# Kernel optimization log

Measured on AMD Instinct MI355X. Metric: run time of the kernel, lower is better.

Reference implementation:

```python
import jax, jax.numpy as jnp
import numpy as np

N_NODES = 250_000
N_EDGES = 4_000_000


def setup_inputs() -> dict:
    key = jax.random.key(0)
    ks = jax.random.split(key, 8)
    x = jax.random.normal(ks[0], (N_NODES, 3), dtype=jnp.float32)
    w = jax.random.normal(ks[1], (N_EDGES, 4), dtype=jnp.float32)
    # MLP params: Linear(10->40), ReLU, Linear(40->4); torch Linear layout [out, in]
    W1 = jax.random.normal(ks[2], (40, 10), dtype=jnp.float32) * (1.0 / np.sqrt(10.0))
    b1 = jax.random.normal(ks[3], (40,), dtype=jnp.float32) * 0.01
    W2 = jax.random.normal(ks[4], (4, 40), dtype=jnp.float32) * (1.0 / np.sqrt(40.0))
    b2 = jax.random.normal(ks[5], (4,), dtype=jnp.float32) * 0.01
    src = jax.random.randint(ks[6], (N_EDGES,), 0, N_NODES, dtype=jnp.int64)
    dst = jax.random.randint(ks[7], (N_EDGES,), 0, N_NODES, dtype=jnp.int64)
    return {"x": x, "w": w, "W1": W1, "b1": b1, "W2": W2, "b2": b2,
            "src": src, "dst": dst}


def reference(x, w, W1, b1, W2, b2, src, dst):
    x_src = x[src]                                  # [E, 3] gather
    x_dst = x[dst]                                  # [E, 3] gather
    m = jnp.concatenate([x_src, x_dst, w], axis=1)  # [E, 10]
    h = jax.nn.relu(m @ W1.T + b1)                  # [E, 40]
    w_out = h @ W2.T + b2                           # [E, 4]
    e_tilde = jnp.concatenate([x_src, w_out], axis=1)  # [E, 7]
    return w_out, e_tilde
```

## Files before the change

kernel.cpp:

```cpp
#include <hip/hip_runtime.h>

typedef __fp16 h2 __attribute__((ext_vector_type(2)));

static __device__ __forceinline__ unsigned pkrtz(float a, float b) {
    union { h2 v; unsigned u; } cv;
    cv.v = __builtin_amdgcn_cvt_pkrtz(a, b);
    return cv.u;
}
static __device__ __forceinline__ h2 as_h2(unsigned u) {
    union { unsigned u; h2 v; } cv; cv.u = u; return cv.v;
}

__global__ void prep_kernel(const float* __restrict__ W1, const float* __restrict__ b1,
                            const float* __restrict__ W2, const float* __restrict__ b2,
                            unsigned* __restrict__ ws) {
    const int t = threadIdx.x;
    if (t < 40) {
        #pragma unroll
        for (int i = 0; i < 5; ++i)
            ws[t * 6 + i] = pkrtz(W1[t * 10 + 2 * i], W1[t * 10 + 2 * i + 1]);
        ws[t * 6 + 5] = __float_as_uint(b1[t]);
    } else if (t < 60) {
        const int p = t - 40;
        #pragma unroll
        for (int o = 0; o < 4; ++o)
            ws[240 + p * 4 + o] = pkrtz(W2[o * 40 + 2 * p], W2[o * 40 + 2 * p + 1]);
    } else if (t < 64) {
        ws[320 + (t - 60)] = __float_as_uint(b2[t - 60]);
    }
}

#define TPB 256

__global__ __launch_bounds__(TPB) void edge_mlp_dot2_kernel(
    const float* __restrict__ x,
    const float* __restrict__ w,
    const int* __restrict__ src,
    const int* __restrict__ dst,
    const unsigned* __restrict__ W,
    float* __restrict__ w_out,
    float* __restrict__ e_tilde,
    int E)
{
    __shared__ float s_et[4][64 * 7];

    const int t    = threadIdx.x;
    const int wave = t >> 6;
    const int lane = t & 63;
    const int e    = blockIdx.x * TPB + t;

    float m0 = 0.f, m1 = 0.f, m2 = 0.f;
    h2 vm0 = as_h2(0), vm1 = as_h2(0), vm2 = as_h2(0), vm3 = as_h2(0), vm4 = as_h2(0);

    if (e < E) {
        const int si = src[e], di = dst[e];
        m0 = x[3 * si]; m1 = x[3 * si + 1]; m2 = x[3 * si + 2];
        const float d0 = x[3 * di], d1 = x[3 * di + 1], d2 = x[3 * di + 2];
        const float4 wv = ((const float4*)w)[e];
        vm0 = as_h2(pkrtz(m0, m1));
        vm1 = as_h2(pkrtz(m2, d0));
        vm2 = as_h2(pkrtz(d1, d2));
        vm3 = as_h2(pkrtz(wv.x, wv.y));
        vm4 = as_h2(pkrtz(wv.z, wv.w));
    }

    float o0 = __uint_as_float(W[320]);
    float o1 = __uint_as_float(W[321]);
    float o2 = __uint_as_float(W[322]);
    float o3 = __uint_as_float(W[323]);

    #pragma unroll
    for (int jp = 0; jp < 20; ++jp) {
        const int j0 = 2 * jp, j1 = 2 * jp + 1;
        float h0v = __uint_as_float(W[j0 * 6 + 5]);
        float h1v = __uint_as_float(W[j1 * 6 + 5]);
        h0v = __builtin_amdgcn_fdot2(vm0, as_h2(W[j0 * 6 + 0]), h0v, false);
        h1v = __builtin_amdgcn_fdot2(vm0, as_h2(W[j1 * 6 + 0]), h1v, false);
        h0v = __builtin_amdgcn_fdot2(vm1, as_h2(W[j0 * 6 + 1]), h0v, false);
        h1v = __builtin_amdgcn_fdot2(vm1, as_h2(W[j1 * 6 + 1]), h1v, false);
        h0v = __builtin_amdgcn_fdot2(vm2, as_h2(W[j0 * 6 + 2]), h0v, false);
        h1v = __builtin_amdgcn_fdot2(vm2, as_h2(W[j1 * 6 + 2]), h1v, false);
        h0v = __builtin_amdgcn_fdot2(vm3, as_h2(W[j0 * 6 + 3]), h0v, false);
        h1v = __builtin_amdgcn_fdot2(vm3, as_h2(W[j1 * 6 + 3]), h1v, false);
        h0v = __builtin_amdgcn_fdot2(vm4, as_h2(W[j0 * 6 + 4]), h0v, false);
        h1v = __builtin_amdgcn_fdot2(vm4, as_h2(W[j1 * 6 + 4]), h1v, false);
        h0v = fmaxf(h0v, 0.f);
        h1v = fmaxf(h1v, 0.f);
        const h2 hp = as_h2(pkrtz(h0v, h1v));
        o0 = __builtin_amdgcn_fdot2(hp, as_h2(W[240 + jp * 4 + 0]), o0, false);
        o1 = __builtin_amdgcn_fdot2(hp, as_h2(W[240 + jp * 4 + 1]), o1, false);
        o2 = __builtin_amdgcn_fdot2(hp, as_h2(W[240 + jp * 4 + 2]), o2, false);
        o3 = __builtin_amdgcn_fdot2(hp, as_h2(W[240 + jp * 4 + 3]), o3, false);
    }

    if (e < E) ((float4*)w_out)[e] = make_float4(o0, o1, o2, o3);

    float* sw = s_et[wave];
    sw[lane * 7 + 0] = m0;
    sw[lane * 7 + 1] = m1;
    sw[lane * 7 + 2] = m2;
    sw[lane * 7 + 3] = o0;
    sw[lane * 7 + 4] = o1;
    sw[lane * 7 + 5] = o2;
    sw[lane * 7 + 6] = o3;
    __syncthreads();

    const int base_e  = blockIdx.x * TPB + wave * 64;
    const int nvalid  = (E - base_e < 64 ? (E - base_e) : 64) * 7;
    const long long fbase = (long long)base_e * 7;
    #pragma unroll
    for (int k = 0; k < 7; ++k) {
        const int idx = lane + 64 * k;
        if (idx < nvalid) e_tilde[fbase + idx] = sw[idx];
    }
}

extern "C" void kernel_launch(void* const* d_in, const int* in_sizes, int n_in,
                              void* d_out, int out_size, void* d_ws, size_t ws_size,
                              hipStream_t stream) {
    const float* x  = (const float*)d_in[0];
    const float* w  = (const float*)d_in[1];
    const float* W1 = (const float*)d_in[2];
    const float* b1 = (const float*)d_in[3];
    const float* W2 = (const float*)d_in[4];
    const float* b2 = (const float*)d_in[5];
    const int* src  = (const int*)d_in[6];
    const int* dst  = (const int*)d_in[7];

    const int E = in_sizes[6];

    float* w_out   = (float*)d_out;
    float* e_tilde = w_out + (size_t)E * 4;
    unsigned* ws   = (unsigned*)d_ws;

    prep_kernel<<<1, 64, 0, stream>>>(W1, b1, W2, b2, ws);

    const int nblocks = (E + TPB - 1) / TPB;
    edge_mlp_dot2_kernel<<<nblocks, TPB, 0, stream>>>(
        x, w, src, dst, ws, w_out, e_tilde, E);
}
```

Measured before the change: 100.3 us.

## Process two edges per thread and write e_tilde directly without LDS staging

Each thread now handles a pair of edges. It loads src/dst as int2, and every loaded weight register feeds two fdot2 computations, which halves the uniform weight loads per edge and adds independent instruction-level parallelism. The shared-memory transpose and __syncthreads are removed; each thread writes its 14 contiguous e_tilde floats as float2 stores. The trade-offs are stride-56-byte per-lane stores with weaker coalescing, more registers per thread, and half as many threads to hide gather latency.

```diff
diff --git a/kernel.cpp b/kernel.cpp
--- a/kernel.cpp
+++ b/kernel.cpp
@@ -32,7 +32,7 @@
 
 #define TPB 256
 
-__global__ __launch_bounds__(TPB) void edge_mlp_dot2_kernel(
+__global__ __launch_bounds__(TPB) void edge_mlp_x2_kernel(
     const float* __restrict__ x,
     const float* __restrict__ w,
     const int* __restrict__ src,
@@ -42,76 +42,123 @@
     float* __restrict__ e_tilde,
     int E)
 {
-    __shared__ float s_et[4][64 * 7];
+    const int g  = blockIdx.x * TPB + threadIdx.x;
+    const int e0 = 2 * g;
+    const bool fa = (e0 < E);
+    const bool fb = (e0 + 1 < E);
 
-    const int t    = threadIdx.x;
-    const int wave = t >> 6;
-    const int lane = t & 63;
-    const int e    = blockIdx.x * TPB + t;
+    float ma0 = 0.f, ma1 = 0.f, ma2 = 0.f;
+    float mb0 = 0.f, mb1 = 0.f, mb2 = 0.f;
+    h2 va0 = as_h2(0), va1 = as_h2(0), va2 = as_h2(0), va3 = as_h2(0), va4 = as_h2(0);
+    h2 vb0 = as_h2(0), vb1 = as_h2(0), vb2 = as_h2(0), vb3 = as_h2(0), vb4 = as_h2(0);
 
-    float m0 = 0.f, m1 = 0.f, m2 = 0.f;
-    h2 vm0 = as_h2(0), vm1 = as_h2(0), vm2 = as_h2(0), vm3 = as_h2(0), vm4 = as_h2(0);
-
-    if (e < E) {
-        const int si = src[e], di = dst[e];
-        m0 = x[3 * si]; m1 = x[3 * si + 1]; m2 = x[3 * si + 2];
-        const float d0 = x[3 * di], d1 = x[3 * di + 1], d2 = x[3 * di + 2];
-        const float4 wv = ((const float4*)w)[e];
-        vm0 = as_h2(pkrtz(m0, m1));
-        vm1 = as_h2(pkrtz(m2, d0));
-        vm2 = as_h2(pkrtz(d1, d2));
-        vm3 = as_h2(pkrtz(wv.x, wv.y));
-        vm4 = as_h2(pkrtz(wv.z, wv.w));
+    if (fb) {
+        const int2 sp = ((const int2*)src)[g];
+        const int2 dp = ((const int2*)dst)[g];
+        const float as0 = x[3 * sp.x], as1 = x[3 * sp.x + 1], as2 = x[3 * sp.x + 2];
+        const float bs0 = x[3 * sp.y], bs1 = x[3 * sp.y + 1], bs2 = x[3 * sp.y + 2];
+        const float ad0 = x[3 * dp.x], ad1 = x[3 * dp.x + 1], ad2 = x[3 * dp.x + 2];
+        const float bd0 = x[3 * dp.y], bd1 = x[3 * dp.y + 1], bd2 = x[3 * dp.y + 2];
+        const float4 wa = ((const float4*)w)[e0];
+        const float4 wb = ((const float4*)w)[e0 + 1];
+        ma0 = as0; ma1 = as1; ma2 = as2;
+        mb0 = bs0; mb1 = bs1; mb2 = bs2;
+        va0 = as_h2(pkrtz(as0, as1)); va1 = as_h2(pkrtz(as2, ad0));
+        va2 = as_h2(pkrtz(ad1, ad2)); va3 = as_h2(pkrtz(wa.x, wa.y));
+        va4 = as_h2(pkrtz(wa.z, wa.w));
+        vb0 = as_h2(pkrtz(bs0, bs1)); vb1 = as_h2(pkrtz(bs2, bd0));
+        vb2 = as_h2(pkrtz(bd1, bd2)); vb3 = as_h2(pkrtz(wb.x, wb.y));
+        vb4 = as_h2(pkrtz(wb.z, wb.w));
+    } else if (fa) {
+        const int si = src[e0], di = dst[e0];
+        const float as0 = x[3 * si], as1 = x[3 * si + 1], as2 = x[3 * si + 2];
+        const float ad0 = x[3 * di], ad1 = x[3 * di + 1], ad2 = x[3 * di + 2];
+        const float4 wa = ((const float4*)w)[e0];
+        ma0 = as0; ma1 = as1; ma2 = as2;
+        va0 = as_h2(pkrtz(as0, as1)); va1 = as_h2(pkrtz(as2, ad0));
+        va2 = as_h2(pkrtz(ad1, ad2)); va3 = as_h2(pkrtz(wa.x, wa.y));
+        va4 = as_h2(pkrtz(wa.z, wa.w));
     }
 
-    float o0 = __uint_as_float(W[320]);
-    float o1 = __uint_as_float(W[321]);
-    float o2 = __uint_as_float(W[322]);
-    float o3 = __uint_as_float(W[323]);
+    float oa0 = __uint_as_float(W[320]);
+    float oa1 = __uint_as_float(W[321]);
+    float oa2 = __uint_as_float(W[322]);
+    float oa3 = __uint_as_float(W[323]);
+    float ob0 = oa0, ob1 = oa1, ob2 = oa2, ob3 = oa3;
 
     #pragma unroll
     for (int jp = 0; jp < 20; ++jp) {
         const int j0 = 2 * jp, j1 = 2 * jp + 1;
-        float h0v = __uint_as_float(W[j0 * 6 + 5]);
-        float h1v = __uint_as_float(W[j1 * 6 + 5]);
-        h0v = __builtin_amdgcn_fdot2(vm0, as_h2(W[j0 * 6 + 0]), h0v, false);
-        h1v = __builtin_amdgcn_fdot2(vm0, as_h2(W[j1 * 6 + 0]), h1v, false);
-        h0v = __builtin_amdgcn_fdot2(vm1, as_h2(W[j0 * 6 + 1]), h0v, false);
-        h1v = __builtin_amdgcn_fdot2(vm1, as_h2(W[j1 * 6 + 1]), h1v, false);
-        h0v = __builtin_amdgcn_fdot2(vm2, as_h2(W[j0 * 6 + 2]), h0v, false);
-        h1v = __builtin_amdgcn_fdot2(vm2, as_h2(W[j1 * 6 + 2]), h1v, false);
-        h0v = __builtin_amdgcn_fdot2(vm3, as_h2(W[j0 * 6 + 3]), h0v, false);
-        h1v = __builtin_amdgcn_fdot2(vm3, as_h2(W[j1 * 6 + 3]), h1v, false);
-        h0v = __builtin_amdgcn_fdot2(vm4, as_h2(W[j0 * 6 + 4]), h0v, false);
-        h1v = __builtin_amdgcn_fdot2(vm4, as_h2(W[j1 * 6 + 4]), h1v, false);
-        h0v = fmaxf(h0v, 0.f);
-        h1v = fmaxf(h1v, 0.f);
-        const h2 hp = as_h2(pkrtz(h0v, h1v));
-        o0 = __builtin_amdgcn_fdot2(hp, as_h2(W[240 + jp * 4 + 0]), o0, false);
-        o1 = __builtin_amdgcn_fdot2(hp, as_h2(W[240 + jp * 4 + 1]), o1, false);
-        o2 = __builtin_amdgcn_fdot2(hp, as_h2(W[240 + jp * 4 + 2]), o2, false);
-        o3 = __builtin_amdgcn_fdot2(hp, as_h2(W[240 + jp * 4 + 3]), o3, false);
+        const h2 w00 = as_h2(W[j0 * 6 + 0]);
+        const h2 w01 = as_h2(W[j0 * 6 + 1]);
+        const h2 w02 = as_h2(W[j0 * 6 + 2]);
+        const h2 w03 = as_h2(W[j0 * 6 + 3]);
+        const h2 w04 = as_h2(W[j0 * 6 + 4]);
+        const h2 w10 = as_h2(W[j1 * 6 + 0]);
+        const h2 w11 = as_h2(W[j1 * 6 + 1]);
+        const h2 w12 = as_h2(W[j1 * 6 + 2]);
+        const h2 w13 = as_h2(W[j1 * 6 + 3]);
+        const h2 w14 = as_h2(W[j1 * 6 + 4]);
+        const float bj0 = __uint_as_float(W[j0 * 6 + 5]);
+        const float bj1 = __uint_as_float(W[j1 * 6 + 5]);
+
+        float h0a = bj0, h1a = bj1, h0b = bj0, h1b = bj1;
+        h0a = __builtin_amdgcn_fdot2(va0, w00, h0a, false);
+        h0b = __builtin_amdgcn_fdot2(vb0, w00, h0b, false);
+        h1a = __builtin_amdgcn_fdot2(va0, w10, h1a, false);
+        h1b = __builtin_amdgcn_fdot2(vb0, w10, h1b, false);
+        h0a = __builtin_amdgcn_fdot2(va1, w01, h0a, false);
+        h0b = __builtin_amdgcn_fdot2(vb1, w01, h0b, false);
+        h1a = __builtin_amdgcn_fdot2(va1, w11, h1a, false);
+        h1b = __builtin_amdgcn_fdot2(vb1, w11, h1b, false);
+        h0a = __builtin_amdgcn_fdot2(va2, w02, h0a, false);
+        h0b = __builtin_amdgcn_fdot2(vb2, w02, h0b, false);
+        h1a = __builtin_amdgcn_fdot2(va2, w12, h1a, false);
+        h1b = __builtin_amdgcn_fdot2(vb2, w12, h1b, false);
+        h0a = __builtin_amdgcn_fdot2(va3, w03, h0a, false);
+        h0b = __builtin_amdgcn_fdot2(vb3, w03, h0b, false);
+        h1a = __builtin_amdgcn_fdot2(va3, w13, h1a, false);
+        h1b = __builtin_amdgcn_fdot2(vb3, w13, h1b, false);
+        h0a = __builtin_amdgcn_fdot2(va4, w04, h0a, false);
+        h0b = __builtin_amdgcn_fdot2(vb4, w04, h0b, false);
+        h1a = __builtin_amdgcn_fdot2(va4, w14, h1a, false);
+        h1b = __builtin_amdgcn_fdot2(vb4, w14, h1b, false);
+
+        h0a = fmaxf(h0a, 0.f); h1a = fmaxf(h1a, 0.f);
+        h0b = fmaxf(h0b, 0.f); h1b = fmaxf(h1b, 0.f);
+        const h2 hpa = as_h2(pkrtz(h0a, h1a));
+        const h2 hpb = as_h2(pkrtz(h0b, h1b));
+
+        const h2 c0 = as_h2(W[240 + jp * 4 + 0]);
+        const h2 c1 = as_h2(W[240 + jp * 4 + 1]);
+        const h2 c2 = as_h2(W[240 + jp * 4 + 2]);
+        const h2 c3 = as_h2(W[240 + jp * 4 + 3]);
+        oa0 = __builtin_amdgcn_fdot2(hpa, c0, oa0, false);
+        ob0 = __builtin_amdgcn_fdot2(hpb, c0, ob0, false);
+        oa1 = __builtin_amdgcn_fdot2(hpa, c1, oa1, false);
+        ob1 = __builtin_amdgcn_fdot2(hpb, c1, ob1, false);
+        oa2 = __builtin_amdgcn_fdot2(hpa, c2, oa2, false);
+        ob2 = __builtin_amdgcn_fdot2(hpb, c2, ob2, false);
+        oa3 = __builtin_amdgcn_fdot2(hpa, c3, oa3, false);
+        ob3 = __builtin_amdgcn_fdot2(hpb, c3, ob3, false);
     }
 
-    if (e < E) ((float4*)w_out)[e] = make_float4(o0, o1, o2, o3);
-
-    float* sw = s_et[wave];
-    sw[lane * 7 + 0] = m0;
-    sw[lane * 7 + 1] = m1;
-    sw[lane * 7 + 2] = m2;
-    sw[lane * 7 + 3] = o0;
-    sw[lane * 7 + 4] = o1;
-    sw[lane * 7 + 5] = o2;
-    sw[lane * 7 + 6] = o3;
-    __syncthreads();
-
-    const int base_e  = blockIdx.x * TPB + wave * 64;
-    const int nvalid  = (E - base_e < 64 ? (E - base_e) : 64) * 7;
-    const long long fbase = (long long)base_e * 7;
-    #pragma unroll
-    for (int k = 0; k < 7; ++k) {
-        const int idx = lane + 64 * k;
-        if (idx < nvalid) e_tilde[fbase + idx] = sw[idx];
+    if (fb) {
+        ((float4*)w_out)[e0]     = make_float4(oa0, oa1, oa2, oa3);
+        ((float4*)w_out)[e0 + 1] = make_float4(ob0, ob1, ob2, ob3);
+        float2* et = (float2*)(e_tilde + (long long)g * 14);
+        et[0] = make_float2(ma0, ma1);
+        et[1] = make_float2(ma2, oa0);
+        et[2] = make_float2(oa1, oa2);
+        et[3] = make_float2(oa3, mb0);
+        et[4] = make_float2(mb1, mb2);
+        et[5] = make_float2(ob0, ob1);
+        et[6] = make_float2(ob2, ob3);
+    } else if (fa) {
+        ((float4*)w_out)[e0] = make_float4(oa0, oa1, oa2, oa3);
+        float* et = e_tilde + (long long)e0 * 7;
+        et[0] = ma0; et[1] = ma1; et[2] = ma2;
+        et[3] = oa0; et[4] = oa1; et[5] = oa2; et[6] = oa3;
     }
 }
 
@@ -135,7 +182,8 @@
 
     prep_kernel<<<1, 64, 0, stream>>>(W1, b1, W2, b2, ws);
 
-    const int nblocks = (E + TPB - 1) / TPB;
-    edge_mlp_dot2_kernel<<<nblocks, TPB, 0, stream>>>(
+    const int npairs  = (E + 1) / 2;
+    const int nblocks = (npairs + TPB - 1) / TPB;
+    edge_mlp_x2_kernel<<<nblocks, TPB, 0, stream>>>(
         x, w, src, dst, ws, w_out, e_tilde, E);
 }
```

New measurement: 111.2 us. 10.9% more time.
